# Kernel optimization log

Hardware: AMD Instinct MI355X
Metric: run time of the kernel (lower is better)

Reference implementation:

```python
import jax, jax.numpy as jnp
import numpy as np

T = 8192          # sequence length
D = 1024          # input_size
H = 16            # n_heads
HEAD = 64         # head_size = hidden_size // n_heads


def setup_inputs() -> dict:
    key = jax.random.key(0)
    ks = jax.random.split(key, 8)
    lim = (1.0 / HEAD) ** 0.5
    u = lambda k, shape: jax.random.uniform(k, shape, minval=-lim, maxval=lim, dtype=jnp.float32)
    return {
        "xs": jax.random.normal(ks[0], (T, D), dtype=jnp.float32),
        "if_weights": u(ks[1], (H, 2, D)),
        "o_weights": u(ks[2], (H, HEAD, D)),
        "kq_weights": u(ks[3], (H, 2 * HEAD, D)),
        "v_weights": u(ks[4], (H, HEAD, D)),
        "if_bias": u(ks[5], (H, 2)),
        "o_bias": u(ks[6], (H, HEAD)),
        "kvq_bias": u(ks[7], (H, 3, HEAD)),
    }


def reference(xs, if_weights, o_weights, kq_weights, v_weights, if_bias, o_bias, kvq_bias):
    inv_sqrt_head = 1.0 / jnp.sqrt(jnp.asarray(HEAD, jnp.float32))

    def step(state, x):
        h_prev, c_prev, m_prev, n_prev = state
        # gates
        i_f = jnp.einsum('htd,d->ht', if_weights, x) + if_bias          # (H, 2)
        o = jax.nn.sigmoid(jnp.einsum('hkd,d->hk', o_weights, x) + o_bias)  # (H, HEAD)
        i, f = i_f[:, 0], i_f[:, 1]
        # log-space stabilizer
        m = jnp.maximum(f + m_prev, i)
        i = jnp.exp(i - m)
        f = jnp.exp(f + m_prev - m)
        # key/query/value projections
        kq = jnp.einsum('hkd,d->hk', kq_weights, x)                      # (H, 2*HEAD)
        k, q = kq[:, :HEAD], kq[:, HEAD:]
        v = jnp.einsum('hkd,d->hk', v_weights, x)
        k = k * inv_sqrt_head + kvq_bias[:, 0]
        v = v + kvq_bias[:, 1]
        q = q + kvq_bias[:, 2]
        # state updates
        n = f[:, None] * n_prev + i[:, None] * k                          # (H, HEAD)
        c = f[:, None, None] * c_prev + i[:, None, None] * (v[:, :, None] * k[:, None, :])  # (H, HEAD, HEAD)
        # readout
        h = jnp.einsum('hij,hj->hi', c, q)                                # (H, HEAD)
        denom = jnp.maximum(jnp.abs(jnp.einsum('hj,hj->h', n, q)), 1.0)  # (H,)
        h = o * (h / denom[:, None])
        return (h, c, m, n), h.reshape(H * HEAD)

    init = (
        jnp.zeros((H, HEAD), jnp.float32),
        jnp.zeros((H, HEAD, HEAD), jnp.float32),
        jnp.zeros((H,), jnp.float32),
        jnp.zeros((H, HEAD), jnp.float32),
    )
    _, hs = jax.lax.scan(step, init, xs)
    return hs  # (T, hidden_size)
```

## Files before the change

### kernel.cpp

```cpp
#include <hip/hip_runtime.h>
#include <math.h>

#define T_LEN 8192
#define D_IN  1024
#define NH    16
#define NPAD  4224
#define NCH   128
#define NGRP  8
#define GSZ   16
#define NPACK 16896
#define NCONV 4096

typedef __attribute__((ext_vector_type(8))) _Float16 f16x8;
typedef __attribute__((ext_vector_type(4))) _Float16 f16x4;
typedef __attribute__((ext_vector_type(4))) float f32x4;

static const size_t OFF_WP   = 0;
static const size_t OFF_BG   = 2300000;
static const size_t OFF_BIAS = OFF_WP + (size_t)NPAD * D_IN;
static const size_t OFF_P    = OFF_BIAS + NPAD;
static const size_t OFF_M    = OFF_P + (size_t)T_LEN * NPAD;
static const size_t OFF_DC   = OFF_M + (size_t)T_LEN * NH;
static const size_t OFF_DN   = OFF_DC + (size_t)NCH * NH * 64 * 64;
static const size_t OFF_DL   = OFF_DN + (size_t)NCH * NH * 64;
static const size_t OFF_IF   = OFF_DL + (size_t)NCH * NH;

__device__ __forceinline__ void glds16(const void* g, void* l) {
  __builtin_amdgcn_global_load_lds(
      (const __attribute__((address_space(1))) void*)g,
      (__attribute__((address_space(3))) void*)l, 16, 0, 0);
}

__global__ __launch_bounds__(256) void pack_conv(
    const float* __restrict__ ifw, const float* __restrict__ ow,
    const float* __restrict__ kqw, const float* __restrict__ vw,
    const float* __restrict__ ifb, const float* __restrict__ ob,
    const float* __restrict__ kvqb, _Float16* __restrict__ Wph,
    float* __restrict__ bias,
    const float* __restrict__ X, _Float16* __restrict__ Xh) {
  int b = blockIdx.x;
  if (b < NPACK) {
    int idx = b * 256 + threadIdx.x;
    int n = idx >> 10, d = idx & 1023;
    float w = 0.f, bb = 0.f;
    if (n < 32) {
      int h = n >> 1, t = n & 1;
      w = ifw[(h * 2 + t) * D_IN + d];
      bb = ifb[h * 2 + t];
    } else if (n < 4128) {
      int r = n - 32;
      int h = r >> 8, j = r & 255;
      if (j < 64)       { w = kqw[(h * 128 + j) * D_IN + d] * 0.125f; bb = kvqb[(h * 3 + 0) * 64 + j]; }
      else if (j < 128) { w = kqw[(h * 128 + j) * D_IN + d];          bb = kvqb[(h * 3 + 2) * 64 + (j - 64)]; }
      else if (j < 192) { w = vw[(h * 64 + (j - 128)) * D_IN + d];    bb = kvqb[(h * 3 + 1) * 64 + (j - 128)]; }
      else              { w = ow[(h * 64 + (j - 192)) * D_IN + d];    bb = ob[h * 64 + (j - 192)]; }
    }
    Wph[(size_t)n * D_IN + d] = (_Float16)w;
    if (d == 0) bias[n] = bb;
  } else {
    int i = ((b - NPACK) * 256 + threadIdx.x) << 3;
    float4 v0 = *(const float4*)(X + i);
    float4 v1 = *(const float4*)(X + i + 4);
    f16x8 r;
    r[0] = (_Float16)v0.x; r[1] = (_Float16)v0.y; r[2] = (_Float16)v0.z; r[3] = (_Float16)v0.w;
    r[4] = (_Float16)v1.x; r[5] = (_Float16)v1.y; r[6] = (_Float16)v1.z; r[7] = (_Float16)v1.w;
    *(f16x8*)(Xh + i) = r;
  }
}

__global__ __launch_bounds__(256) void gemm_f16(
    const _Float16* __restrict__ Xh, const _Float16* __restrict__ Wph,
    const float* __restrict__ bias, _Float16* __restrict__ Ph) {
  __shared__ _Float16 As[3][128 * 32];
  __shared__ _Float16 Bs[3][128 * 32];
  int tid = threadIdx.x;
  int wave = tid >> 6, lane = tid & 63;
  int wgid = blockIdx.x;
  int virt = (wgid & 7) * 264 + (wgid >> 3);
  int mt = virt / 33, nt = virt % 33;
  int m0 = mt << 7, n0 = nt << 7;
  int wr = wave >> 1, wc = wave & 1;

  f32x4 acc[4][4];
  f32x4 zero = {0.f, 0.f, 0.f, 0.f};
#pragma unroll
  for (int i = 0; i < 4; ++i)
#pragma unroll
    for (int j = 0; j < 4; ++j) acc[i][j] = zero;

  int srow = lane >> 2;
  int scol = (((lane & 3) ^ ((lane >> 3) & 3)) << 3);
  const _Float16* ga = Xh + (size_t)(m0 + wave * 32 + srow) * D_IN + scol;
  const _Float16* gb = Wph + (size_t)(n0 + wave * 32 + srow) * D_IN + scol;
  int lds0 = (wave * 32) * 32;
  int lds1 = (wave * 32 + 16) * 32;

  int fr = lane & 15;
  int fko = (((lane >> 4) ^ ((fr >> 1) & 3)) << 3);

#define STG(T, S) do { int ko_ = (T) << 5;                         \
    glds16(ga + ko_, &As[S][lds0]);                                \
    glds16(ga + 16 * D_IN + ko_, &As[S][lds1]);                    \
    glds16(gb + ko_, &Bs[S][lds0]);                                \
    glds16(gb + 16 * D_IN + ko_, &Bs[S][lds1]);                    \
  } while (0)

  STG(0, 0);
  STG(1, 1);

  int slot = 0;
  for (int i = 0; i < 32; ++i) {
    if (i < 31) asm volatile("s_waitcnt vmcnt(4)" ::: "memory");
    else        asm volatile("s_waitcnt vmcnt(0)" ::: "memory");
    __builtin_amdgcn_s_barrier();
    __builtin_amdgcn_sched_barrier(0);
    if (i < 30) {
      int ns = slot + 2; if (ns >= 3) ns -= 3;
      STG(i + 2, ns);
    }
    f16x8 a[4], b[4];
#pragma unroll
    for (int mi = 0; mi < 4; ++mi)
      a[mi] = *(const f16x8*)&As[slot][(wr * 64 + mi * 16 + fr) * 32 + fko];
#pragma unroll
    for (int ni = 0; ni < 4; ++ni)
      b[ni] = *(const f16x8*)&Bs[slot][(wc * 64 + ni * 16 + fr) * 32 + fko];
    __builtin_amdgcn_s_setprio(1);
#pragma unroll
    for (int mi = 0; mi < 4; ++mi)
#pragma unroll
      for (int ni = 0; ni < 4; ++ni)
        acc[mi][ni] = __builtin_amdgcn_mfma_f32_16x16x32_f16(a[mi], b[ni], acc[mi][ni], 0, 0, 0);
    __builtin_amdgcn_s_setprio(0);
    slot = slot + 1; if (slot >= 3) slot = 0;
  }
#undef STG

  int cr = (lane >> 4) << 2;
  int cc = lane & 15;
#pragma unroll
  for (int mi = 0; mi < 4; ++mi) {
#pragma unroll
    for (int ni = 0; ni < 4; ++ni) {
      int col = n0 + wc * 64 + ni * 16 + cc;
      float bb = bias[col];
      size_t base = (size_t)(m0 + wr * 64 + mi * 16 + cr) * NPAD + col;
#pragma unroll
      for (int r = 0; r < 4; ++r)
        Ph[base + (size_t)r * NPAD] = (_Float16)(acc[mi][ni][r] + bb);
    }
  }
}

__global__ __launch_bounds__(256) void gemm_if(
    const float* __restrict__ X, const float* __restrict__ ifw,
    const float* __restrict__ ifb, float* __restrict__ IFc) {
  __shared__ float Xs[32 * 72];
  __shared__ float Ws[32 * 68];
  int tid = threadIdx.x;
  int r0 = blockIdx.x << 5;
  int nc = tid & 15;
  int rg = tid >> 4;
  int n0 = nc << 1;
  int sw = ((n0 >> 3) & 3) << 2;
  int sx = ((rg >> 1) & 3) << 2;

  float acc[2][2];
  acc[0][0] = acc[0][1] = acc[1][0] = acc[1][1] = 0.f;

  for (int k0 = 0; k0 < D_IN; k0 += 64) {
    __syncthreads();
#pragma unroll
    for (int i = 0; i < 2; ++i) {
      int fi = (i << 8) + tid;
      int row = fi >> 4, kk = (fi & 15) << 2;
      float4 v = *(const float4*)(X + (size_t)(r0 + row) * D_IN + k0 + kk);
      *(float4*)&Xs[row * 72 + (kk ^ (((row >> 2) & 3) << 2))] = v;
    }
#pragma unroll
    for (int i = 0; i < 2; ++i) {
      int fi = (i << 8) + tid;
      int row = fi >> 4, kk = (fi & 15) << 2;
      float4 v = *(const float4*)(ifw + (size_t)row * D_IN + k0 + kk);
      *(float4*)&Ws[row * 68 + (kk ^ (((row >> 3) & 3) << 2))] = v;
    }
    __syncthreads();
#pragma unroll
    for (int k4 = 0; k4 < 64; k4 += 4) {
      float4 w0 = *(const float4*)&Ws[n0 * 68 + (k4 ^ sw)];
      float4 w1 = *(const float4*)&Ws[(n0 + 1) * 68 + (k4 ^ sw)];
#pragma unroll
      for (int j = 0; j < 2; ++j) {
        float4 xv = *(const float4*)&Xs[((rg << 1) + j) * 72 + (k4 ^ sx)];
        acc[j][0] = fmaf(xv.x, w0.x, acc[j][0]);
        acc[j][0] = fmaf(xv.y, w0.y, acc[j][0]);
        acc[j][0] = fmaf(xv.z, w0.z, acc[j][0]);
        acc[j][0] = fmaf(xv.w, w0.w, acc[j][0]);
        acc[j][1] = fmaf(xv.x, w1.x, acc[j][1]);
        acc[j][1] = fmaf(xv.y, w1.y, acc[j][1]);
        acc[j][1] = fmaf(xv.z, w1.z, acc[j][1]);
        acc[j][1] = fmaf(xv.w, w1.w, acc[j][1]);
      }
    }
  }
  float b0 = ifb[n0], b1 = ifb[n0 + 1];
#pragma unroll
  for (int j = 0; j < 2; ++j) {
    int row = r0 + (rg << 1) + j;
    float2 st; st.x = acc[j][0] + b0; st.y = acc[j][1] + b1;
    *(float2*)(IFc + ((size_t)row << 5) + n0) = st;
  }
}

__global__ __launch_bounds__(256) void mscan(const float* __restrict__ IFc, float* __restrict__ M) {
  int h = blockIdx.x;
  int tid = threadIdx.x;
  int lane = tid & 63, wv = tid >> 6;
  int t0 = tid << 5;
  float F = 0.f, I = -1e30f;
#pragma unroll 8
  for (int u = 0; u < 32; ++u) {
    float2 v = *(const float2*)(IFc + ((size_t)(t0 + u) << 5) + (h << 1));
    I = fmaxf(I + v.y, v.x);
    F += v.y;
  }
#pragma unroll
  for (int d = 1; d < 64; d <<= 1) {
    float Fo = __shfl_up(F, d, 64);
    float Io = __shfl_up(I, d, 64);
    if (lane >= d) { I = fmaxf(Io + F, I); F = Fo + F; }
  }
  __shared__ float sF[4], sI[4];
  if (lane == 63) { sF[wv] = F; sI[wv] = I; }
  float Fe = __shfl_up(F, 1, 64);
  float Ie = __shfl_up(I, 1, 64);
  if (lane == 0) { Fe = 0.f; Ie = -1e30f; }
  __syncthreads();
  float Fp = 0.f, Ip = -1e30f;
  for (int w = 0; w < wv; ++w) { Ip = fmaxf(Ip + sF[w], sI[w]); Fp += sF[w]; }
  float Ft = Fp + Fe;
  float It = fmaxf(Ip + Fe, Ie);
  float m = fmaxf(Ft, It);
#pragma unroll 8
  for (int u = 0; u < 32; ++u) {
    float2 v = *(const float2*)(IFc + ((size_t)(t0 + u) << 5) + (h << 1));
    m = fmaxf(v.y + m, v.x);
    M[(size_t)(t0 + u) * NH + h] = m;
  }
}

__global__ __launch_bounds__(256) void d1_dc(
    const _Float16* __restrict__ Ph, const float* __restrict__ IFc,
    const float* __restrict__ M,
    _Float16* __restrict__ DCh, float* __restrict__ DN, float* __restrict__ DL) {
  int c = blockIdx.x >> 4, h = blockIdx.x & 15;
  int t0 = c << 6, hb = 32 + (h << 8);
  int tid = threadIdx.x;
  int lane = tid & 63, wave = tid >> 6;
  __shared__ _Float16 Kt[64 * 72];
  __shared__ _Float16 Vt[64 * 72];
  __shared__ float gl[64];
#pragma unroll
  for (int i = 0; i < 2; ++i) {
    int fq = (i << 8) + tid;
    int s = fq >> 3, b8 = (fq & 7) << 3;
    const _Float16* row = Ph + (size_t)(t0 + s) * NPAD + hb;
    f16x8 kv = *(const f16x8*)(row + b8);
    f16x8 vv = *(const f16x8*)(row + 128 + b8);
#pragma unroll
    for (int j = 0; j < 8; ++j) {
      Kt[(b8 + j) * 72 + s] = kv[j];
      Vt[(b8 + j) * 72 + s] = vv[j];
    }
  }
  if (tid < 64) {
    float2 iff = *(const float2*)(IFc + ((size_t)(t0 + tid) << 5) + (h << 1));
    float iv = iff.x, fv = iff.y;
    float cs = fv;
#pragma unroll
    for (int dd = 1; dd < 64; dd <<= 1) {
      float o = __shfl_up(cs, dd, 64);
      cs += (tid >= dd) ? o : 0.f;
    }
    float cumL = __shfl(cs, 63, 64);
    float mL = M[(size_t)(t0 + 63) * NH + h];
    gl[tid] = __expf(cumL - cs + iv - mL);
    if (tid == 0) {
      float mstart = (c > 0) ? M[(size_t)(t0 - 1) * NH + h] : 0.f;
      DL[(c << 4) + h] = __expf(mstart + cumL - mL);
    }
  }
  __syncthreads();
  if (tid < 64) {
    float acc = 0.f;
#pragma unroll
    for (int s = 0; s < 64; ++s) acc = fmaf(gl[s], (float)Kt[tid * 72 + s], acc);
    DN[((size_t)(c << 4) + h) * 64 + tid] = acc;
  }
  int arow = lane & 15;
  int kq = (lane >> 4) << 3;
  int aR = (wave << 4) + arow;
  f16x8 ag0, ag1;
#pragma unroll
  for (int j = 0; j < 8; ++j) {
    ag0[j] = (_Float16)(gl[kq + j] * (float)Vt[aR * 72 + kq + j]);
    ag1[j] = (_Float16)(gl[32 + kq + j] * (float)Vt[aR * 72 + 32 + kq + j]);
  }
  f32x4 accD[4];
  f32x4 zero = {0.f, 0.f, 0.f, 0.f};
#pragma unroll
  for (int n = 0; n < 4; ++n) accD[n] = zero;
#pragma unroll
  for (int n = 0; n < 4; ++n) {
    f16x8 b0 = *(const f16x8*)&Kt[((n << 4) + arow) * 72 + kq];
    f16x8 b1 = *(const f16x8*)&Kt[((n << 4) + arow) * 72 + 32 + kq];
    accD[n] = __builtin_amdgcn_mfma_f32_16x16x32_f16(ag0, b0, accD[n], 0, 0, 0);
    accD[n] = __builtin_amdgcn_mfma_f32_16x16x32_f16(ag1, b1, accD[n], 0, 0, 0);
  }
  __syncthreads();
  int crow = (lane >> 4) << 2, cc = lane & 15;
#pragma unroll
  for (int n = 0; n < 4; ++n)
#pragma unroll
    for (int r = 0; r < 4; ++r)
      Vt[((wave << 4) + crow + r) * 72 + (n << 4) + cc] = (_Float16)accD[n][r];
  __syncthreads();
  size_t base = ((size_t)(c << 4) + h) << 12;
#pragma unroll
  for (int i = 0; i < 2; ++i) {
    int fq = (i << 8) + tid;
    int a = fq >> 3, b8 = (fq & 7) << 3;
    *(f16x8*)(DCh + base + ((size_t)a << 6) + b8) = *(const f16x8*)&Vt[a * 72 + b8];
  }
}

__global__ __launch_bounds__(256) void d2a(
    const _Float16* __restrict__ DCh, const float* __restrict__ DN,
    const float* __restrict__ DL,
    float* __restrict__ BgDC, float* __restrict__ BgDN, float* __restrict__ Ag) {
  int bid = blockIdx.x, tid = threadIdx.x;
  if (bid < 2048) {
    int linear = (bid << 8) + tid;
    int g = linear >> 16, e = linear & 65535;
    int h = e >> 12;
    float carry = 0.f, a = 1.f;
    size_t idx = (size_t)e + ((size_t)g << 4) * 65536;
    float v = (float)DCh[idx];
    for (int u = 0; u < GSZ; ++u) {
      float dl = DL[(((g << 4) + u) << 4) + h];
      float vn = (u < GSZ - 1) ? (float)DCh[idx + 65536] : 0.f;
      carry = fmaf(dl, carry, v);
      a *= dl;
      v = vn;
      idx += 65536;
    }
    BgDC[((size_t)g << 16) + e] = carry;
    if ((e & 4095) == 0) Ag[(g << 4) + h] = a;
  } else {
    int linear = ((bid - 2048) << 8) + tid;
    int g = linear >> 10, e = linear & 1023;
    int h = e >> 6;
    float carry = 0.f;
    size_t idx = (size_t)e + ((size_t)g << 4) * 1024;
    float v = DN[idx];
    for (int u = 0; u < GSZ; ++u) {
      float dl = DL[(((g << 4) + u) << 4) + h];
      float vn = (u < GSZ - 1) ? DN[idx + 1024] : 0.f;
      carry = fmaf(dl, carry, v);
      v = vn;
      idx += 1024;
    }
    BgDN[(g << 10) + e] = carry;
  }
}

__global__ __launch_bounds__(256) void d2c(
    _Float16* __restrict__ DCh, float* __restrict__ DN,
    const float* __restrict__ DL,
    const float* __restrict__ BgDC, const float* __restrict__ BgDN,
    const float* __restrict__ Ag) {
  int bid = blockIdx.x, tid = threadIdx.x;
  if (bid < 2048) {
    int linear = (bid << 8) + tid;
    int g = linear >> 16, e = linear & 65535;
    int h = e >> 12;
    float P = 0.f;
    for (int gp = 0; gp < g; ++gp)
      P = fmaf(Ag[(gp << 4) + h], P, BgDC[((size_t)gp << 16) + e]);
    float carry = P;
    size_t idx = (size_t)e + ((size_t)g << 4) * 65536;
    float v = (float)DCh[idx];
    for (int u = 0; u < GSZ; ++u) {
      float dl = DL[(((g << 4) + u) << 4) + h];
      float vn = (u < GSZ - 1) ? (float)DCh[idx + 65536] : 0.f;
      DCh[idx] = (_Float16)carry;
      carry = fmaf(dl, carry, v);
      v = vn;
      idx += 65536;
    }
  } else {
    int linear = ((bid - 2048) << 8) + tid;
    int g = linear >> 10, e = linear & 1023;
    int h = e >> 6;
    float P = 0.f;
    for (int gp = 0; gp < g; ++gp)
      P = fmaf(Ag[(gp << 4) + h], P, BgDN[(gp << 10) + e]);
    float carry = P;
    size_t idx = (size_t)e + ((size_t)g << 4) * 1024;
    float v = DN[idx];
    for (int u = 0; u < GSZ; ++u) {
      float dl = DL[(((g << 4) + u) << 4) + h];
      float vn = (u < GSZ - 1) ? DN[idx + 1024] : 0.f;
      DN[idx] = carry;
      carry = fmaf(dl, carry, v);
      v = vn;
      idx += 1024;
    }
  }
}

__global__ __launch_bounds__(256) void d3_out(
    const _Float16* __restrict__ Ph, const float* __restrict__ IFc,
    const float* __restrict__ M,
    const _Float16* __restrict__ CS, const float* __restrict__ NS,
    float* __restrict__ out) {
  int c = blockIdx.x >> 4, h = blockIdx.x & 15;
  int t0 = c << 6, hb = 32 + (h << 8);
  int tid = threadIdx.x;
  int lane = tid & 63, wave = tid >> 6;
  __shared__ _Float16 Kh[64 * 72];
  __shared__ _Float16 Qh[64 * 72];
  __shared__ _Float16 Vt[64 * 72];
  __shared__ _Float16 Ch[64 * 72];
  __shared__ _Float16 Oh[64 * 72];
  __shared__ _Float16 Pl[64 * 72];
  __shared__ float cf[64], il[64], ml[64], dl[64], nq[64], nsl[64];

#pragma unroll
  for (int i = 0; i < 2; ++i) {
    int fq = (i << 8) + tid;
    int s = fq >> 3, b8 = (fq & 7) << 3;
    const _Float16* row = Ph + (size_t)(t0 + s) * NPAD + hb;
    f16x8 kv = *(const f16x8*)(row + b8);
    f16x8 qv = *(const f16x8*)(row + 64 + b8);
    f16x8 vv = *(const f16x8*)(row + 128 + b8);
    f16x8 ov = *(const f16x8*)(row + 192 + b8);
    f16x8 cv = *(const f16x8*)(CS + ((((size_t)(c << 4)) + h) << 12) + ((size_t)s << 6) + b8);
    *(f16x8*)&Kh[s * 72 + b8] = kv;
    *(f16x8*)&Qh[s * 72 + b8] = qv;
    *(f16x8*)&Oh[s * 72 + b8] = ov;
    *(f16x8*)&Ch[s * 72 + b8] = cv;
#pragma unroll
    for (int j = 0; j < 8; ++j) Vt[(b8 + j) * 72 + s] = vv[j];
  }
  __syncthreads();

  float iv = 0.f, mt = 0.f, cs = 0.f;
  if (tid < 64) {
    float2 iff = *(const float2*)(IFc + ((size_t)(t0 + tid) << 5) + (h << 1));
    iv = iff.x;
    float fv = iff.y;
    mt = M[(size_t)(t0 + tid) * NH + h];
    nsl[tid] = NS[((size_t)(c << 4) + h) * 64 + tid];
    cs = fv;
#pragma unroll
    for (int dd = 1; dd < 64; dd <<= 1) {
      float o = __shfl_up(cs, dd, 64);
      cs += (tid >= dd) ? o : 0.f;
    }
  }
  __syncthreads();
  if (tid < 64) {
    cf[tid] = cs; il[tid] = iv; ml[tid] = mt;
    float mstart = (c > 0) ? M[(size_t)(t0 - 1) * NH + h] : 0.f;
    dl[tid] = __expf(mstart + cs - mt);
    float acc = 0.f;
#pragma unroll
    for (int b = 0; b < 64; ++b) acc = fmaf(nsl[b], (float)Qh[tid * 72 + b], acc);
    nq[tid] = acc;
  }
  __syncthreads();

  int band = wave << 4;
  int arow = lane & 15;
  int kq = (lane >> 4) << 3;
  int crow = (lane >> 4) << 2;

  f16x8 aq0 = *(const f16x8*)&Qh[(band + arow) * 72 + kq];
  f16x8 aq1 = *(const f16x8*)&Qh[(band + arow) * 72 + 32 + kq];

  f32x4 S[4];
  f32x4 zero = {0.f, 0.f, 0.f, 0.f};
#pragma unroll
  for (int n = 0; n < 4; ++n) S[n] = zero;
#pragma unroll
  for (int n = 0; n < 4; ++n) {
    f16x8 b0 = *(const f16x8*)&Kh[((n << 4) + arow) * 72 + kq];
    f16x8 b1 = *(const f16x8*)&Kh[((n << 4) + arow) * 72 + 32 + kq];
    S[n] = __builtin_amdgcn_mfma_f32_16x16x32_f16(aq0, b0, S[n], 0, 0, 0);
    S[n] = __builtin_amdgcn_mfma_f32_16x16x32_f16(aq1, b1, S[n], 0, 0, 0);
  }

  float cft[4], mlt[4];
#pragma unroll
  for (int r = 0; r < 4; ++r) {
    int t = band + crow + r;
    cft[r] = cf[t]; mlt[r] = ml[t];
  }
  float rsum[4] = {0.f, 0.f, 0.f, 0.f};
#pragma unroll
  for (int n = 0; n < 4; ++n) {
    int s = (n << 4) + arow;
    float cfs = cf[s], ils = il[s];
#pragma unroll
    for (int r = 0; r < 4; ++r) {
      int t = band + crow + r;
      float w = (s <= t) ? __expf(cft[r] - cfs + ils - mlt[r]) : 0.f;
      float p = S[n][r] * w;
      rsum[r] += p;
      Pl[t * 72 + s] = (_Float16)p;
    }
  }
#pragma unroll
  for (int r = 0; r < 4; ++r) {
    float p = rsum[r];
    p += __shfl_xor(p, 1);
    p += __shfl_xor(p, 2);
    p += __shfl_xor(p, 4);
    p += __shfl_xor(p, 8);
    rsum[r] = p;
  }
  __syncthreads();

  f16x8 ap0 = *(const f16x8*)&Pl[(band + arow) * 72 + kq];
  f16x8 ap1 = *(const f16x8*)&Pl[(band + arow) * 72 + 32 + kq];
  f32x4 H[4], I[4];
#pragma unroll
  for (int n = 0; n < 4; ++n) { H[n] = zero; I[n] = zero; }
#pragma unroll
  for (int n = 0; n < 4; ++n) {
    f16x8 bv0 = *(const f16x8*)&Vt[((n << 4) + arow) * 72 + kq];
    f16x8 bv1 = *(const f16x8*)&Vt[((n << 4) + arow) * 72 + 32 + kq];
    H[n] = __builtin_amdgcn_mfma_f32_16x16x32_f16(ap0, bv0, H[n], 0, 0, 0);
    H[n] = __builtin_amdgcn_mfma_f32_16x16x32_f16(ap1, bv1, H[n], 0, 0, 0);
    f16x8 bc0 = *(const f16x8*)&Ch[((n << 4) + arow) * 72 + kq];
    f16x8 bc1 = *(const f16x8*)&Ch[((n << 4) + arow) * 72 + 32 + kq];
    I[n] = __builtin_amdgcn_mfma_f32_16x16x32_f16(aq0, bc0, I[n], 0, 0, 0);
    I[n] = __builtin_amdgcn_mfma_f32_16x16x32_f16(aq1, bc1, I[n], 0, 0, 0);
  }

#pragma unroll
  for (int r = 0; r < 4; ++r) {
    int t = band + crow + r;
    float dt = dl[t];
    float dn = fmaf(dt, nq[t], rsum[r]);
    float rinv = 1.f / fmaxf(fabsf(dn), 1.f);
    float* orow = out + (size_t)(t0 + t) * 1024 + (h << 6);
#pragma unroll
    for (int n = 0; n < 4; ++n) {
      int a = (n << 4) + arow;
      float o = 1.f / (1.f + __expf(-(float)Oh[t * 72 + a]));
      orow[a] = o * (fmaf(dt, I[n][r], H[n][r]) * rinv);
    }
  }
}

extern "C" void kernel_launch(void* const* d_in, const int* in_sizes, int n_in,
                              void* d_out, int out_size, void* d_ws, size_t ws_size,
                              hipStream_t stream) {
  const float* xs   = (const float*)d_in[0];
  const float* ifw  = (const float*)d_in[1];
  const float* ow   = (const float*)d_in[2];
  const float* kqw  = (const float*)d_in[3];
  const float* vw   = (const float*)d_in[4];
  const float* ifb  = (const float*)d_in[5];
  const float* ob   = (const float*)d_in[6];
  const float* kvqb = (const float*)d_in[7];
  float* ws   = (float*)d_ws;
  _Float16* Wph = (_Float16*)(ws + OFF_WP);
  float* BgDC = ws + OFF_BG;
  float* BgDN = BgDC + (size_t)NGRP * 65536;
  float* Ag   = BgDN + (size_t)NGRP * 1024;
  float* bias = ws + OFF_BIAS;
  _Float16* Phm = (_Float16*)(ws + OFF_P);
  float* Mm   = ws + OFF_M;
  _Float16* DCh = (_Float16*)(ws + OFF_DC);
  _Float16* Xh  = (_Float16*)(ws + OFF_DC);
  float* DN   = ws + OFF_DN;
  float* DL   = ws + OFF_DL;
  float* IFc  = ws + OFF_IF;
  float* outp = (float*)d_out;

  hipLaunchKernelGGL(pack_conv, dim3(NPACK + NCONV), dim3(256), 0, stream,
                     ifw, ow, kqw, vw, ifb, ob, kvqb, Wph, bias, xs, Xh);
  hipLaunchKernelGGL(gemm_f16, dim3(33 * 64), dim3(256), 0, stream,
                     Xh, Wph, bias, Phm);
  hipLaunchKernelGGL(gemm_if, dim3(T_LEN / 32), dim3(256), 0, stream, xs, ifw, ifb, IFc);
  hipLaunchKernelGGL(mscan, dim3(NH), dim3(256), 0, stream, IFc, Mm);
  hipLaunchKernelGGL(d1_dc, dim3(NCH * NH), dim3(256), 0, stream, Phm, IFc, Mm, DCh, DN, DL);
  hipLaunchKernelGGL(d2a, dim3(2080), dim3(256), 0, stream, DCh, DN, DL, BgDC, BgDN, Ag);
  hipLaunchKernelGGL(d2c, dim3(2080), dim3(256), 0, stream, DCh, DN, DL, BgDC, BgDN, Ag);
  hipLaunchKernelGGL(d3_out, dim3(NCH * NH), dim3(256), 0, stream, Phm, IFc, Mm, DCh, DN, outp);
}
```

Before: 215.6 us.

## Fuse gate GEMM into main GEMM launch and parallelize small dot products

Merges the f16 projection GEMM and the fp32 input/forget-gate GEMM into one launch, with block ranges selecting the path, to remove a launch and let the two overlap. The main GEMM drops its three-stage LDS pipeline with vmcnt waits for a double buffer with __syncthreads, which shrinks shared memory but may expose more load latency. The per-row 64-length dot products in d1_dc and d3_out now use all 256 threads with shuffle reductions instead of 64 threads. d3_out reuses the K buffer for P, adding a barrier, and reads the output-gate values straight from global memory instead of staging them in LDS, which cuts shared memory use.

```diff
diff --git a/kernel.cpp b/kernel.cpp
--- a/kernel.cpp
+++ b/kernel.cpp
@@ -10,6 +10,7 @@
 #define GSZ   16
 #define NPACK 16896
 #define NCONV 4096
+#define NGEMM 2112
 
 typedef __attribute__((ext_vector_type(8))) _Float16 f16x8;
 typedef __attribute__((ext_vector_type(4))) _Float16 f16x4;
@@ -68,147 +69,144 @@
   }
 }
 
-__global__ __launch_bounds__(256) void gemm_f16(
+__global__ __launch_bounds__(256) void gemm_fused(
     const _Float16* __restrict__ Xh, const _Float16* __restrict__ Wph,
-    const float* __restrict__ bias, _Float16* __restrict__ Ph) {
-  __shared__ _Float16 As[3][128 * 32];
-  __shared__ _Float16 Bs[3][128 * 32];
-  int tid = threadIdx.x;
-  int wave = tid >> 6, lane = tid & 63;
-  int wgid = blockIdx.x;
-  int virt = (wgid & 7) * 264 + (wgid >> 3);
-  int mt = virt / 33, nt = virt % 33;
-  int m0 = mt << 7, n0 = nt << 7;
-  int wr = wave >> 1, wc = wave & 1;
-
-  f32x4 acc[4][4];
-  f32x4 zero = {0.f, 0.f, 0.f, 0.f};
-#pragma unroll
-  for (int i = 0; i < 4; ++i)
-#pragma unroll
-    for (int j = 0; j < 4; ++j) acc[i][j] = zero;
-
-  int srow = lane >> 2;
-  int scol = (((lane & 3) ^ ((lane >> 3) & 3)) << 3);
-  const _Float16* ga = Xh + (size_t)(m0 + wave * 32 + srow) * D_IN + scol;
-  const _Float16* gb = Wph + (size_t)(n0 + wave * 32 + srow) * D_IN + scol;
-  int lds0 = (wave * 32) * 32;
-  int lds1 = (wave * 32 + 16) * 32;
-
-  int fr = lane & 15;
-  int fko = (((lane >> 4) ^ ((fr >> 1) & 3)) << 3);
-
-#define STG(T, S) do { int ko_ = (T) << 5;                         \
-    glds16(ga + ko_, &As[S][lds0]);                                \
-    glds16(ga + 16 * D_IN + ko_, &As[S][lds1]);                    \
-    glds16(gb + ko_, &Bs[S][lds0]);                                \
-    glds16(gb + 16 * D_IN + ko_, &Bs[S][lds1]);                    \
-  } while (0)
-
-  STG(0, 0);
-  STG(1, 1);
-
-  int slot = 0;
-  for (int i = 0; i < 32; ++i) {
-    if (i < 31) asm volatile("s_waitcnt vmcnt(4)" ::: "memory");
-    else        asm volatile("s_waitcnt vmcnt(0)" ::: "memory");
-    __builtin_amdgcn_s_barrier();
-    __builtin_amdgcn_sched_barrier(0);
-    if (i < 30) {
-      int ns = slot + 2; if (ns >= 3) ns -= 3;
-      STG(i + 2, ns);
-    }
-    f16x8 a[4], b[4];
-#pragma unroll
-    for (int mi = 0; mi < 4; ++mi)
-      a[mi] = *(const f16x8*)&As[slot][(wr * 64 + mi * 16 + fr) * 32 + fko];
-#pragma unroll
-    for (int ni = 0; ni < 4; ++ni)
-      b[ni] = *(const f16x8*)&Bs[slot][(wc * 64 + ni * 16 + fr) * 32 + fko];
-    __builtin_amdgcn_s_setprio(1);
-#pragma unroll
-    for (int mi = 0; mi < 4; ++mi)
-#pragma unroll
-      for (int ni = 0; ni < 4; ++ni)
-        acc[mi][ni] = __builtin_amdgcn_mfma_f32_16x16x32_f16(a[mi], b[ni], acc[mi][ni], 0, 0, 0);
-    __builtin_amdgcn_s_setprio(0);
-    slot = slot + 1; if (slot >= 3) slot = 0;
-  }
-#undef STG
-
-  int cr = (lane >> 4) << 2;
-  int cc = lane & 15;
-#pragma unroll
-  for (int mi = 0; mi < 4; ++mi) {
-#pragma unroll
-    for (int ni = 0; ni < 4; ++ni) {
-      int col = n0 + wc * 64 + ni * 16 + cc;
-      float bb = bias[col];
-      size_t base = (size_t)(m0 + wr * 64 + mi * 16 + cr) * NPAD + col;
-#pragma unroll
-      for (int r = 0; r < 4; ++r)
-        Ph[base + (size_t)r * NPAD] = (_Float16)(acc[mi][ni][r] + bb);
-    }
-  }
-}
-
-__global__ __launch_bounds__(256) void gemm_if(
+    const float* __restrict__ bias, _Float16* __restrict__ Ph,
     const float* __restrict__ X, const float* __restrict__ ifw,
     const float* __restrict__ ifb, float* __restrict__ IFc) {
-  __shared__ float Xs[32 * 72];
-  __shared__ float Ws[32 * 68];
+  __shared__ __align__(16) char smem[32768];
   int tid = threadIdx.x;
-  int r0 = blockIdx.x << 5;
-  int nc = tid & 15;
-  int rg = tid >> 4;
-  int n0 = nc << 1;
-  int sw = ((n0 >> 3) & 3) << 2;
-  int sx = ((rg >> 1) & 3) << 2;
-
-  float acc[2][2];
-  acc[0][0] = acc[0][1] = acc[1][0] = acc[1][1] = 0.f;
-
-  for (int k0 = 0; k0 < D_IN; k0 += 64) {
+  if (blockIdx.x < NGEMM) {
+    _Float16* As = (_Float16*)smem;
+    _Float16* Bs = (_Float16*)(smem + 16384);
+    int wave = tid >> 6, lane = tid & 63;
+    int wgid = blockIdx.x;
+    int virt = (wgid & 7) * 264 + (wgid >> 3);
+    int mt = virt / 33, nt = virt % 33;
+    int m0 = mt << 7, n0 = nt << 7;
+    int wr = wave >> 1, wc = wave & 1;
+
+    f32x4 acc[4][4];
+    f32x4 zero = {0.f, 0.f, 0.f, 0.f};
+#pragma unroll
+    for (int i = 0; i < 4; ++i)
+#pragma unroll
+      for (int j = 0; j < 4; ++j) acc[i][j] = zero;
+
+    int srow = lane >> 2;
+    int scol = (((lane & 3) ^ ((lane >> 3) & 3)) << 3);
+    const _Float16* ga = Xh + (size_t)(m0 + wave * 32 + srow) * D_IN + scol;
+    const _Float16* gb = Wph + (size_t)(n0 + wave * 32 + srow) * D_IN + scol;
+    int lds0 = (wave * 32) * 32;
+    int lds1 = (wave * 32 + 16) * 32;
+
+    int fr = lane & 15;
+    int fko = (((lane >> 4) ^ ((fr >> 1) & 3)) << 3);
+
+    glds16(ga, &As[lds0]);
+    glds16(ga + 16 * D_IN, &As[lds1]);
+    glds16(gb, &Bs[lds0]);
+    glds16(gb + 16 * D_IN, &Bs[lds1]);
     __syncthreads();
-#pragma unroll
-    for (int i = 0; i < 2; ++i) {
-      int fi = (i << 8) + tid;
-      int row = fi >> 4, kk = (fi & 15) << 2;
-      float4 v = *(const float4*)(X + (size_t)(r0 + row) * D_IN + k0 + kk);
-      *(float4*)&Xs[row * 72 + (kk ^ (((row >> 2) & 3) << 2))] = v;
-    }
-#pragma unroll
-    for (int i = 0; i < 2; ++i) {
-      int fi = (i << 8) + tid;
-      int row = fi >> 4, kk = (fi & 15) << 2;
-      float4 v = *(const float4*)(ifw + (size_t)row * D_IN + k0 + kk);
-      *(float4*)&Ws[row * 68 + (kk ^ (((row >> 3) & 3) << 2))] = v;
-    }
-    __syncthreads();
-#pragma unroll
-    for (int k4 = 0; k4 < 64; k4 += 4) {
-      float4 w0 = *(const float4*)&Ws[n0 * 68 + (k4 ^ sw)];
-      float4 w1 = *(const float4*)&Ws[(n0 + 1) * 68 + (k4 ^ sw)];
-#pragma unroll
-      for (int j = 0; j < 2; ++j) {
-        float4 xv = *(const float4*)&Xs[((rg << 1) + j) * 72 + (k4 ^ sx)];
-        acc[j][0] = fmaf(xv.x, w0.x, acc[j][0]);
-        acc[j][0] = fmaf(xv.y, w0.y, acc[j][0]);
-        acc[j][0] = fmaf(xv.z, w0.z, acc[j][0]);
-        acc[j][0] = fmaf(xv.w, w0.w, acc[j][0]);
-        acc[j][1] = fmaf(xv.x, w1.x, acc[j][1]);
-        acc[j][1] = fmaf(xv.y, w1.y, acc[j][1]);
-        acc[j][1] = fmaf(xv.z, w1.z, acc[j][1]);
-        acc[j][1] = fmaf(xv.w, w1.w, acc[j][1]);
+
+    int cur = 0;
+    for (int k0 = 0; k0 < D_IN; k0 += 32) {
+      if (k0 + 32 < D_IN) {
+        int kn = k0 + 32;
+        int other = (cur ^ 1) * 4096;
+        glds16(ga + kn, &As[other + lds0]);
+        glds16(ga + 16 * D_IN + kn, &As[other + lds1]);
+        glds16(gb + kn, &Bs[other + lds0]);
+        glds16(gb + 16 * D_IN + kn, &Bs[other + lds1]);
       }
-    }
-  }
-  float b0 = ifb[n0], b1 = ifb[n0 + 1];
-#pragma unroll
-  for (int j = 0; j < 2; ++j) {
-    int row = r0 + (rg << 1) + j;
-    float2 st; st.x = acc[j][0] + b0; st.y = acc[j][1] + b1;
-    *(float2*)(IFc + ((size_t)row << 5) + n0) = st;
+      int cb = cur * 4096;
+      f16x8 a[4], b[4];
+#pragma unroll
+      for (int mi = 0; mi < 4; ++mi)
+        a[mi] = *(const f16x8*)&As[cb + (wr * 64 + mi * 16 + fr) * 32 + fko];
+#pragma unroll
+      for (int ni = 0; ni < 4; ++ni)
+        b[ni] = *(const f16x8*)&Bs[cb + (wc * 64 + ni * 16 + fr) * 32 + fko];
+      __builtin_amdgcn_s_setprio(1);
+#pragma unroll
+      for (int mi = 0; mi < 4; ++mi)
+#pragma unroll
+        for (int ni = 0; ni < 4; ++ni)
+          acc[mi][ni] = __builtin_amdgcn_mfma_f32_16x16x32_f16(a[mi], b[ni], acc[mi][ni], 0, 0, 0);
+      __builtin_amdgcn_s_setprio(0);
+      __syncthreads();
+      cur ^= 1;
+    }
+
+    int cr = (lane >> 4) << 2;
+    int cc = lane & 15;
+#pragma unroll
+    for (int mi = 0; mi < 4; ++mi) {
+#pragma unroll
+      for (int ni = 0; ni < 4; ++ni) {
+        int col = n0 + wc * 64 + ni * 16 + cc;
+        float bb = bias[col];
+        size_t base = (size_t)(m0 + wr * 64 + mi * 16 + cr) * NPAD + col;
+#pragma unroll
+        for (int r = 0; r < 4; ++r)
+          Ph[base + (size_t)r * NPAD] = (_Float16)(acc[mi][ni][r] + bb);
+      }
+    }
+  } else {
+    float* Xs = (float*)smem;
+    float* Ws = (float*)(smem + 9216);
+    int r0 = (blockIdx.x - NGEMM) << 5;
+    int nc = tid & 15;
+    int rg = tid >> 4;
+    int n0 = nc << 1;
+    int sw = ((n0 >> 3) & 3) << 2;
+    int sx = ((rg >> 1) & 3) << 2;
+
+    float acc[2][2];
+    acc[0][0] = acc[0][1] = acc[1][0] = acc[1][1] = 0.f;
+
+    for (int k0 = 0; k0 < D_IN; k0 += 64) {
+      __syncthreads();
+#pragma unroll
+      for (int i = 0; i < 2; ++i) {
+        int fi = (i << 8) + tid;
+        int row = fi >> 4, kk = (fi & 15) << 2;
+        float4 v = *(const float4*)(X + (size_t)(r0 + row) * D_IN + k0 + kk);
+        *(float4*)&Xs[row * 72 + (kk ^ (((row >> 2) & 3) << 2))] = v;
+      }
+#pragma unroll
+      for (int i = 0; i < 2; ++i) {
+        int fi = (i << 8) + tid;
+        int row = fi >> 4, kk = (fi & 15) << 2;
+        float4 v = *(const float4*)(ifw + (size_t)row * D_IN + k0 + kk);
+        *(float4*)&Ws[row * 68 + (kk ^ (((row >> 3) & 3) << 2))] = v;
+      }
+      __syncthreads();
+#pragma unroll
+      for (int k4 = 0; k4 < 64; k4 += 4) {
+        float4 w0 = *(const float4*)&Ws[n0 * 68 + (k4 ^ sw)];
+        float4 w1 = *(const float4*)&Ws[(n0 + 1) * 68 + (k4 ^ sw)];
+#pragma unroll
+        for (int j = 0; j < 2; ++j) {
+          float4 xv = *(const float4*)&Xs[((rg << 1) + j) * 72 + (k4 ^ sx)];
+          acc[j][0] = fmaf(xv.x, w0.x, acc[j][0]);
+          acc[j][0] = fmaf(xv.y, w0.y, acc[j][0]);
+          acc[j][0] = fmaf(xv.z, w0.z, acc[j][0]);
+          acc[j][0] = fmaf(xv.w, w0.w, acc[j][0]);
+          acc[j][1] = fmaf(xv.x, w1.x, acc[j][1]);
+          acc[j][1] = fmaf(xv.y, w1.y, acc[j][1]);
+          acc[j][1] = fmaf(xv.z, w1.z, acc[j][1]);
+          acc[j][1] = fmaf(xv.w, w1.w, acc[j][1]);
+        }
+      }
+    }
+    float b0 = ifb[n0], b1 = ifb[n0 + 1];
+#pragma unroll
+    for (int j = 0; j < 2; ++j) {
+      int row = r0 + (rg << 1) + j;
+      float2 st; st.x = acc[j][0] + b0; st.y = acc[j][1] + b1;
+      *(float2*)(IFc + ((size_t)row << 5) + n0) = st;
+    }
   }
 }
 
@@ -291,11 +289,15 @@
     }
   }
   __syncthreads();
-  if (tid < 64) {
-    float acc = 0.f;
-#pragma unroll
-    for (int s = 0; s < 64; ++s) acc = fmaf(gl[s], (float)Kt[tid * 72 + s], acc);
-    DN[((size_t)(c << 4) + h) * 64 + tid] = acc;
+  {
+    int b = tid >> 2, seg = (tid & 3) << 4;
+    float part = 0.f;
+#pragma unroll
+    for (int j = 0; j < 16; ++j)
+      part = fmaf(gl[seg + j], (float)Kt[b * 72 + seg + j], part);
+    part += __shfl_xor(part, 1);
+    part += __shfl_xor(part, 2);
+    if ((tid & 3) == 0) DN[((size_t)(c << 4) + h) * 64 + b] = part;
   }
   int arow = lane & 15;
   int kq = (lane >> 4) << 3;
@@ -432,8 +434,6 @@
   __shared__ _Float16 Qh[64 * 72];
   __shared__ _Float16 Vt[64 * 72];
   __shared__ _Float16 Ch[64 * 72];
-  __shared__ _Float16 Oh[64 * 72];
-  __shared__ _Float16 Pl[64 * 72];
   __shared__ float cf[64], il[64], ml[64], dl[64], nq[64], nsl[64];
 
 #pragma unroll
@@ -444,11 +444,9 @@
     f16x8 kv = *(const f16x8*)(row + b8);
     f16x8 qv = *(const f16x8*)(row + 64 + b8);
     f16x8 vv = *(const f16x8*)(row + 128 + b8);
-    f16x8 ov = *(const f16x8*)(row + 192 + b8);
     f16x8 cv = *(const f16x8*)(CS + ((((size_t)(c << 4)) + h) << 12) + ((size_t)s << 6) + b8);
     *(f16x8*)&Kh[s * 72 + b8] = kv;
     *(f16x8*)&Qh[s * 72 + b8] = qv;
-    *(f16x8*)&Oh[s * 72 + b8] = ov;
     *(f16x8*)&Ch[s * 72 + b8] = cv;
 #pragma unroll
     for (int j = 0; j < 8; ++j) Vt[(b8 + j) * 72 + s] = vv[j];
@@ -474,10 +472,16 @@
     cf[tid] = cs; il[tid] = iv; ml[tid] = mt;
     float mstart = (c > 0) ? M[(size_t)(t0 - 1) * NH + h] : 0.f;
     dl[tid] = __expf(mstart + cs - mt);
-    float acc = 0.f;
-#pragma unroll
-    for (int b = 0; b < 64; ++b) acc = fmaf(nsl[b], (float)Qh[tid * 72 + b], acc);
-    nq[tid] = acc;
+  }
+  {
+    int r = tid >> 2, seg = (tid & 3) << 4;
+    float part = 0.f;
+#pragma unroll
+    for (int j = 0; j < 16; ++j)
+      part = fmaf(nsl[seg + j], (float)Qh[r * 72 + seg + j], part);
+    part += __shfl_xor(part, 1);
+    part += __shfl_xor(part, 2);
+    if ((tid & 3) == 0) nq[r] = part;
   }
   __syncthreads();
 
@@ -500,6 +504,7 @@
     S[n] = __builtin_amdgcn_mfma_f32_16x16x32_f16(aq0, b0, S[n], 0, 0, 0);
     S[n] = __builtin_amdgcn_mfma_f32_16x16x32_f16(aq1, b1, S[n], 0, 0, 0);
   }
+  __syncthreads();
 
   float cft[4], mlt[4];
 #pragma unroll
@@ -518,7 +523,7 @@
       float w = (s <= t) ? __expf(cft[r] - cfs + ils - mlt[r]) : 0.f;
       float p = S[n][r] * w;
       rsum[r] += p;
-      Pl[t * 72 + s] = (_Float16)p;
+      Kh[t * 72 + s] = (_Float16)p;
     }
   }
 #pragma unroll
@@ -532,8 +537,8 @@
   }
   __syncthreads();
 
-  f16x8 ap0 = *(const f16x8*)&Pl[(band + arow) * 72 + kq];
-  f16x8 ap1 = *(const f16x8*)&Pl[(band + arow) * 72 + 32 + kq];
+  f16x8 ap0 = *(const f16x8*)&Kh[(band + arow) * 72 + kq];
+  f16x8 ap1 = *(const f16x8*)&Kh[(band + arow) * 72 + 32 + kq];
   f32x4 H[4], I[4];
 #pragma unroll
   for (int n = 0; n < 4; ++n) { H[n] = zero; I[n] = zero; }
@@ -556,10 +561,11 @@
     float dn = fmaf(dt, nq[t], rsum[r]);
     float rinv = 1.f / fmaxf(fabsf(dn), 1.f);
     float* orow = out + (size_t)(t0 + t) * 1024 + (h << 6);
+    const _Float16* og = Ph + (size_t)(t0 + t) * NPAD + hb + 192;
 #pragma unroll
     for (int n = 0; n < 4; ++n) {
       int a = (n << 4) + arow;
-      float o = 1.f / (1.f + __expf(-(float)Oh[t * 72 + a]));
+      float o = 1.f / (1.f + __expf(-(float)og[a]));
       orow[a] = o * (fmaf(dt, I[n][r], H[n][r]) * rinv);
     }
   }
@@ -593,9 +599,8 @@
 
   hipLaunchKernelGGL(pack_conv, dim3(NPACK + NCONV), dim3(256), 0, stream,
                      ifw, ow, kqw, vw, ifb, ob, kvqb, Wph, bias, xs, Xh);
-  hipLaunchKernelGGL(gemm_f16, dim3(33 * 64), dim3(256), 0, stream,
-                     Xh, Wph, bias, Phm);
-  hipLaunchKernelGGL(gemm_if, dim3(T_LEN / 32), dim3(256), 0, stream, xs, ifw, ifb, IFc);
+  hipLaunchKernelGGL(gemm_fused, dim3(NGEMM + 256), dim3(256), 0, stream,
+                     Xh, Wph, bias, Phm, xs, ifw, ifb, IFc);
   hipLaunchKernelGGL(mscan, dim3(NH), dim3(256), 0, stream, IFc, Mm);
   hipLaunchKernelGGL(d1_dc, dim3(NCH * NH), dim3(256), 0, stream, Phm, IFc, Mm, DCh, DN, DL);
   hipLaunchKernelGGL(d2a, dim3(2080), dim3(256), 0, stream, DCh, DN, DL, BgDC, BgDN, Ag);
```

After: 216.2 us. About the same (+0.2%).
